# Optimization experiments

Hardware: AMD Instinct MI355X
Metric: run time of the kernel (lower is better)

## Reference

```python
import jax, jax.numpy as jnp
import numpy as np

N = 50000; E = 800000; G = 64
HID = 128; HEADS = 4; HC = HID // HEADS
L = 3; RESID_FREQ = 2
EPS = 1e-5; SLOPE = 0.2


def setup_inputs() -> dict:
    key = jax.random.key(0)
    ks = jax.random.split(key, 16)
    s = 1.0 / np.sqrt(HID)
    f = jnp.float32
    return {
        "x": jax.random.normal(ks[0], (N, HID), f),
        "edge_index": jax.random.randint(ks[1], (2, E), 0, N, dtype=jnp.int32),
        "batch": jnp.sort(jax.random.randint(ks[2], (N,), 0, G, dtype=jnp.int32)),
        "w_in1": jax.random.normal(ks[3], (HID, HID), f) * s,
        "b_in1": jnp.zeros((HID,), f),
        "w_in2": jax.random.normal(ks[4], (HID, HID), f) * s,
        "b_in2": jnp.zeros((HID,), f),
        "gat_w": jax.random.normal(ks[5], (L, HID, HID), f) * s,
        "gat_att_src": jax.random.normal(ks[6], (L, HEADS, HC), f) * s,
        "gat_att_dst": jax.random.normal(ks[7], (L, HEADS, HC), f) * s,
        "gat_b": jnp.zeros((L, HID), f),
        "gcn_w": jax.random.normal(ks[8], (L, HID, HID), f) * s,
        "gcn_b": jnp.zeros((L, HID), f),
        "norm_w": jnp.ones((L, HID), f),
        "norm_b": jnp.zeros((L, HID), f),
        "norm_ms": jnp.ones((L, HID), f),
        "skip_w": jax.random.normal(ks[9], (L, HID, HID), f) * s,
        "skip_b": jnp.zeros((L, HID), f),
        "w_h1": jax.random.normal(ks[10], (HID, HID), f) * s,
        "b_h1": jnp.zeros((HID,), f),
        "w_h2": jax.random.normal(ks[11], (HID, HID // 2), f) * s,
        "b_h2": jnp.zeros((HID // 2,), f),
        "w_h3": jax.random.normal(ks[12], (HID // 2, 1), f) * s,
        "b_h3": jnp.zeros((1,), f),
        "edge_w_param": jnp.ones((1,), f),
    }


def _gat(x, src, dst, w, a_src, a_dst, b):
    # PyG GATConv (eval): lin -> per-edge additive attention -> edge softmax over dst -> scatter-sum
    h = (x @ w).reshape(N, HEADS, HC)
    sc_src = jnp.sum(h * a_src, axis=-1)  # [N, H]
    sc_dst = jnp.sum(h * a_dst, axis=-1)
    alpha = jax.nn.leaky_relu(sc_src[src] + sc_dst[dst], SLOPE)  # [Ef, H]
    amax = jax.ops.segment_max(alpha, dst, num_segments=N)  # every node has a self-loop
    ex = jnp.exp(alpha - amax[dst])
    denom = jax.ops.segment_sum(ex, dst, num_segments=N)
    coef = ex / (denom[dst] + 1e-16)
    out = jax.ops.segment_sum(h[src] * coef[:, :, None], dst, num_segments=N)
    return out.reshape(N, HID) + b


def _gcn(x, src, dst, ew, w, b):
    # PyG GCNConv with improved=True (self-loop weight 2.0 already in ew): sym-normalized SpMM
    deg = jax.ops.segment_sum(ew, dst, num_segments=N)
    dinv = jnp.where(deg > 0, jax.lax.rsqrt(deg), 0.0)
    norm = dinv[src] * ew * dinv[dst]
    h = x @ w
    return jax.ops.segment_sum(h[src] * norm[:, None], dst, num_segments=N) + b


def _graph_norm(x, batch, w, b, ms):
    cnt = jax.ops.segment_sum(jnp.ones((N, 1), x.dtype), batch, num_segments=G)
    cnt = jnp.maximum(cnt, 1.0)
    mean = jax.ops.segment_sum(x, batch, num_segments=G) / cnt
    out = x - mean[batch] * ms
    var = jax.ops.segment_sum(out * out, batch, num_segments=G) / cnt
    return out / jnp.sqrt(var[batch] + EPS) * w + b


def reference(x, edge_index, batch, w_in1, b_in1, w_in2, b_in2, gat_w, gat_att_src,
              gat_att_dst, gat_b, gcn_w, gcn_b, norm_w, norm_b, norm_ms, skip_w,
              skip_b, w_h1, b_h1, w_h2, b_h2, w_h3, b_h3, edge_w_param):
    # undirected: concat reversed edges; then self-loops (added by both GAT and GCN convs)
    loop = jnp.arange(N, dtype=edge_index.dtype)
    src = jnp.concatenate([edge_index[0], edge_index[1], loop])
    dst = jnp.concatenate([edge_index[1], edge_index[0], loop])
    ew = jnp.concatenate([
        edge_w_param[0] * jnp.ones((2 * E,), x.dtype),
        2.0 * jnp.ones((N,), x.dtype),  # improved=True self-loop fill value
    ])
    h = jax.nn.relu(x @ w_in1 + b_in1) @ w_in2 + b_in2
    for i in range(L):
        prev = h
        g1 = _gat(h, src, dst, gat_w[i], gat_att_src[i], gat_att_dst[i], gat_b[i])
        g2 = _gcn(h, src, dst, ew, gcn_w[i], gcn_b[i])
        h = jax.nn.elu(_graph_norm(g1 + g2, batch, norm_w[i], norm_b[i], norm_ms[i]))
        if i % RESID_FREQ == 0:
            h = h + prev @ skip_w[i] + skip_b[i]
    p = jax.nn.relu(h @ w_h1 + b_h1)
    p = jax.nn.relu(p @ w_h2 + b_h2)
    return jax.nn.sigmoid(p @ w_h3 + b_h3).reshape(-1)
```

## Files before the change

### kernel.cpp

```cpp
#include <hip/hip_runtime.h>

typedef unsigned int uint;
typedef unsigned short ushort;
typedef __attribute__((ext_vector_type(8))) short short8;
typedef __attribute__((ext_vector_type(4))) float f32x4;

#define N_NODES 50000
#define N_EDGES 800000
#define ETOT    (2 * N_EDGES + N_NODES)
#define NG      64
#define NBKT    256
#define MAXB    10240
#define EPB     8192
#define NBK1    ((ETOT + EPB - 1) / EPB)
#define GSTR    320

__device__ __forceinline__ short f2bf(float f) {
  uint u = __float_as_uint(f);
  u += 0x7fffu + ((u >> 16) & 1u);
  return (short)(u >> 16);
}
__device__ __forceinline__ float bf2f(short s) {
  return __uint_as_float(((uint)(ushort)s) << 16);
}
__device__ __forceinline__ uint packbf(float a, float b) {
  return (uint)(ushort)f2bf(a) | ((uint)(ushort)f2bf(b) << 16);
}

__global__ __launch_bounds__(256) void bucket_k(const int* __restrict__ ei,
                                                int* __restrict__ gfill,
                                                uint* __restrict__ est) {
  __shared__ int hist[NBKT];
  __shared__ int cursor[NBKT];
  const int tid = threadIdx.x;
  hist[tid] = 0;
  __syncthreads();
  const int e0 = blockIdx.x * EPB;
#pragma unroll 4
  for (int i = 0; i < EPB / 256; ++i) {
    int e = e0 + i * 256 + tid;
    if (e < ETOT) {
      int d;
      if (e < N_EDGES)          d = ei[N_EDGES + e];
      else if (e < 2 * N_EDGES) d = ei[e - N_EDGES];
      else                      d = e - 2 * N_EDGES;
      atomicAdd(&hist[d >> 8], 1);
    }
  }
  __syncthreads();
  cursor[tid] = atomicAdd(&gfill[tid], hist[tid]);
  __syncthreads();
#pragma unroll 4
  for (int i = 0; i < EPB / 256; ++i) {
    int e = e0 + i * 256 + tid;
    if (e < ETOT) {
      int s, d, fl = 0;
      if (e < N_EDGES)          { s = ei[e];           d = ei[N_EDGES + e]; }
      else if (e < 2 * N_EDGES) { s = ei[e];           d = ei[e - N_EDGES]; }
      else                      { s = e - 2 * N_EDGES; d = s; fl = 1; }
      int b = d >> 8;
      int slot = atomicAdd(&cursor[b], 1);
      est[(size_t)b * MAXB + slot] = (uint)s | ((uint)(d & 255) << 16) | ((uint)fl << 24);
    }
  }
}

__global__ __launch_bounds__(256) void group_k(const int* __restrict__ gfill,
                                               const uint* __restrict__ est,
                                               const float* __restrict__ ewp,
                                               int* __restrict__ csrc,
                                               int* __restrict__ rbeg,
                                               int* __restrict__ rend,
                                               float* __restrict__ dinv) {
  __shared__ int hist[NBKT];
  __shared__ int cursor[NBKT];
  __shared__ int wsum[4];
  const int b = blockIdx.x;
  const int tid = threadIdx.x;
  const int cnt = gfill[b];
  hist[tid] = 0;
  __syncthreads();
  const uint* basep = est + (size_t)b * MAXB;
  for (int i = tid; i < cnt; i += 256)
    atomicAdd(&hist[(basep[i] >> 16) & 255], 1);
  __syncthreads();
  int v = hist[tid];
  int lane = tid & 63, wid = tid >> 6;
  int x = v;
#pragma unroll
  for (int d = 1; d < 64; d <<= 1) {
    int t = __shfl_up(x, d, 64);
    if (lane >= d) x += t;
  }
  if (lane == 63) wsum[wid] = x;
  __syncthreads();
  int woff = 0;
#pragma unroll
  for (int j = 0; j < 4; ++j) if (j < wid) woff += wsum[j];
  int excl = woff + x - v;
  cursor[tid] = excl;
  int node = b * 256 + tid;
  if (node < N_NODES) {
    int gb = b * MAXB;
    rbeg[node] = gb + excl;
    rend[node] = gb + excl + v;
    float deg = ewp[0] * (float)(v - 1) + 2.0f;
    dinv[node] = (deg > 0.f) ? rsqrtf(deg) : 0.f;
  }
  __syncthreads();
  for (int i = tid; i < cnt; i += 256) {
    uint en = basep[i];
    int dlow = (en >> 16) & 255;
    int slot = atomicAdd(&cursor[dlow], 1);
    csrc[(size_t)b * MAXB + slot] = (int)(en & 0xffffu) | (int)((en >> 24) << 31);
  }
}

__global__ __launch_bounds__(128) void gcnt_k(const int* __restrict__ batch,
                                              int* __restrict__ gcnt) {
  __shared__ int lb[NG + 1];
  int g = threadIdx.x;
  if (g <= NG) {
    int lo = 0, hi = N_NODES;
    while (lo < hi) {
      int mid = (lo + hi) >> 1;
      if (batch[mid] < g) lo = mid + 1; else hi = mid;
    }
    lb[g] = lo;
  }
  __syncthreads();
  if (g < NG) gcnt[g] = lb[g + 1] - lb[g];
}

__global__ __launch_bounds__(256) void convx_k(const float* __restrict__ x,
                                               short* __restrict__ xb) {
  int i = (blockIdx.x * 256 + threadIdx.x) * 4;
  float4 v = *(const float4*)(x + i);
  *(uint2*)(xb + i) = make_uint2(packbf(v.x, v.y), packbf(v.z, v.w));
}

__global__ __launch_bounds__(256) void prep_k(const float* __restrict__ w_in1,
                                              const float* __restrict__ w_in2,
                                              const float* __restrict__ gat_w,
                                              const float* __restrict__ gcn_w,
                                              const float* __restrict__ skip_w,
                                              const float* __restrict__ w_h1,
                                              const float* __restrict__ w_h2,
                                              short* __restrict__ WT0,
                                              short* __restrict__ WT1,
                                              short* __restrict__ WTL2,
                                              short* __restrict__ WTS,
                                              short* __restrict__ WTH1,
                                              short* __restrict__ WTH2) {
  int mat = blockIdx.x >> 2, qr = blockIdx.x & 3;
  const float* src; short* dst; int ncol = 128, dstride = 128, doff = 0;
  switch (mat) {
    case 0:  src = w_in1; dst = WT0; break;
    case 1:  src = w_in2; dst = WT1; break;
    case 2: case 3: case 4:
      src = gat_w + (size_t)(mat - 2) * 16384; dst = WTL2 + (size_t)(mat - 2) * 32768;
      dstride = 256; break;
    case 5: case 6: case 7:
      src = gcn_w + (size_t)(mat - 5) * 16384; dst = WTL2 + (size_t)(mat - 5) * 32768;
      dstride = 256; doff = 128; break;
    case 8:  src = skip_w;             dst = WTS;         break;
    case 9:  src = skip_w + 2 * 16384; dst = WTS + 16384; break;
    case 10: src = w_h1; dst = WTH1; break;
    default: src = w_h2; dst = WTH2; ncol = 64; break;
  }
  int total = 128 * ncol, chunk = total / 4;
  for (int d = qr * chunk + threadIdx.x; d < (qr + 1) * chunk; d += 256) {
    int col = d >> 7, k = d & 127;
    dst[col * dstride + doff + k] = f2bf(src[k * ncol + col]);
  }
}

__global__ __launch_bounds__(256) void attprep_k(const float* __restrict__ gat_w,
                                                 const float* __restrict__ asrc,
                                                 const float* __restrict__ adst,
                                                 const float* __restrict__ gat_b,
                                                 const float* __restrict__ gcn_b,
                                                 short* __restrict__ ATTW,
                                                 float* __restrict__ BSUM) {
  const int tid = threadIdx.x;
  for (int t = tid; t < 3072; t += 256) {
    int l = t >> 10, rem = t & 1023;
    int r = rem >> 7, k = rem & 127;
    int hd = r & 3;
    const float* av = (r < 4) ? (asrc + l * 128 + hd * 32) : (adst + l * 128 + hd * 32);
    const float* wrow = gat_w + (size_t)l * 16384 + k * 128 + hd * 32;
    float s = 0.f;
#pragma unroll
    for (int c = 0; c < 32; ++c) s = fmaf(wrow[c], av[c], s);
    ATTW[(size_t)l * 2048 + r * 128 + k] = f2bf(s);
  }
  for (int t = tid; t < 3072; t += 256)
    ATTW[(size_t)(t >> 10) * 2048 + 1024 + (t & 1023)] = 0;
  for (int t = tid; t < 384; t += 256) {
    int l = t >> 7, c = t & 127;
    BSUM[t] = gat_b[l * 128 + c] + gcn_b[l * 128 + c];
  }
}

template <int NCOL, int RELU, int ADD, int F32OUT>
__global__ __launch_bounds__(256) void bgemm_k(const short* __restrict__ A,
                                               const short* __restrict__ WT,
                                               const float* __restrict__ bias,
                                               const float* __restrict__ addsrc,
                                               short* __restrict__ outb,
                                               float* __restrict__ outf,
                                               int astr, int M) {
  constexpr int NT = NCOL / 16;
  const int lane = threadIdx.x & 63;
  const int wid = threadIdx.x >> 6;
  const int mbase = blockIdx.x * 64 + wid * 16;
  const int l15 = lane & 15, q = lane >> 4;
  int arow = mbase + l15; if (arow > M - 1) arow = M - 1;
  const short* ap = A + (size_t)arow * 128 + q * 8;
  const short* bp = WT + (size_t)l15 * 128 + q * 8;
  f32x4 acc[NT];
#pragma unroll
  for (int t = 0; t < NT; ++t) acc[t] = (f32x4)0.f;
#pragma unroll
  for (int c = 0; c < 4; ++c) {
    short8 av = *(const short8*)(ap + c * 32);
#pragma unroll
    for (int t = 0; t < NT; ++t) {
      short8 bv = *(const short8*)(bp + (size_t)t * 16 * 128 + c * 32);
      acc[t] = __builtin_amdgcn_mfma_f32_16x16x32_bf16(av, bv, acc[t], 0, 0, 0);
    }
  }
#pragma unroll
  for (int t = 0; t < NT; ++t) {
    int col = t * 16 + l15;
    float bb = bias ? bias[col] : 0.f;
#pragma unroll
    for (int r = 0; r < 4; ++r) {
      int row = mbase + q * 4 + r;
      if (row < M) {
        float v = acc[t][r] + bb;
        if (ADD) v += addsrc[(size_t)row * astr + col];
        if (RELU) v = v > 0.f ? v : 0.f;
        if (F32OUT) outf[(size_t)row * NCOL + col] = v;
        else        outb[(size_t)row * NCOL + col] = f2bf(v);
      }
    }
  }
}

__global__ __launch_bounds__(256) void agg_k(const short* __restrict__ h,
                                             const float* __restrict__ sc,
                                             const int* __restrict__ rbeg,
                                             const int* __restrict__ rend,
                                             const int* __restrict__ cs,
                                             const float* __restrict__ dinv,
                                             const float* __restrict__ ewp,
                                             short* __restrict__ A) {
  const int n = blockIdx.x * 4 + (threadIdx.x >> 6);
  const int l = threadIdx.x & 63;
  const int sub = l >> 5;
  const int f4 = l & 31;
  const float ew0 = ewp[0];
  const f32x4 sdv = *(const f32x4*)(sc + n * 16 + 4);
  const float dn = dinv[n];
  const int beg = rbeg[n], end = rend[n];
  float den[4] = {0.f, 0.f, 0.f, 0.f};
  float ag[4][4];
#pragma unroll
  for (int hd = 0; hd < 4; ++hd)
#pragma unroll
    for (int i = 0; i < 4; ++i) ag[hd][i] = 0.f;
  float ac[4] = {0.f, 0.f, 0.f, 0.f};
  for (int e0 = beg; e0 < end; e0 += 2) {
    int e = e0 + sub;
    bool valid = e < end;
    int ec = valid ? e : end - 1;
    int raw = cs[ec];
    int s = raw & 0x7fffffff;
    float w = (raw < 0) ? 2.0f : ew0;
    f32x4 ssv = *(const f32x4*)(sc + s * 16);
    float dvs = dinv[s];
    uint2 u = *(const uint2*)(h + (size_t)s * 128 + f4 * 4);
    float c2 = valid ? dvs * w * dn : 0.f;
    float v0 = __uint_as_float(u.x << 16);
    float v1 = __uint_as_float(u.x & 0xffff0000u);
    float v2 = __uint_as_float(u.y << 16);
    float v3 = __uint_as_float(u.y & 0xffff0000u);
#pragma unroll
    for (int hd = 0; hd < 4; ++hd) {
      float al = ssv[hd] + sdv[hd];
      al = fmaxf(al, 0.2f * al);
      float ex = valid ? __expf(al) : 0.f;
      den[hd] += ex;
      ag[hd][0] = fmaf(ex, v0, ag[hd][0]);
      ag[hd][1] = fmaf(ex, v1, ag[hd][1]);
      ag[hd][2] = fmaf(ex, v2, ag[hd][2]);
      ag[hd][3] = fmaf(ex, v3, ag[hd][3]);
    }
    ac[0] = fmaf(c2, v0, ac[0]);
    ac[1] = fmaf(c2, v1, ac[1]);
    ac[2] = fmaf(c2, v2, ac[2]);
    ac[3] = fmaf(c2, v3, ac[3]);
  }
#pragma unroll
  for (int hd = 0; hd < 4; ++hd) {
    den[hd] += __shfl_xor(den[hd], 32);
#pragma unroll
    for (int i = 0; i < 4; ++i) ag[hd][i] += __shfl_xor(ag[hd][i], 32);
  }
#pragma unroll
  for (int i = 0; i < 4; ++i) ac[i] += __shfl_xor(ac[i], 32);
  short* base = A + (size_t)n * 640;
  if (sub == 0) {
#pragma unroll
    for (int hd = 0; hd < 2; ++hd) {
      float inv = 1.0f / (den[hd] + 1e-16f);
      *(uint2*)(base + hd * 128 + f4 * 4) =
          make_uint2(packbf(ag[hd][0] * inv, ag[hd][1] * inv),
                     packbf(ag[hd][2] * inv, ag[hd][3] * inv));
    }
    *(uint2*)(base + 512 + f4 * 4) =
        make_uint2(packbf(ac[0], ac[1]), packbf(ac[2], ac[3]));
  } else {
#pragma unroll
    for (int hd = 2; hd < 4; ++hd) {
      float inv = 1.0f / (den[hd] + 1e-16f);
      *(uint2*)(base + hd * 128 + f4 * 4) =
          make_uint2(packbf(ag[hd][0] * inv, ag[hd][1] * inv),
                     packbf(ag[hd][2] * inv, ag[hd][3] * inv));
    }
  }
}

__global__ __launch_bounds__(256) void aggproj_k(const short* A,
                                                 const short* __restrict__ WT,
                                                 const float* __restrict__ bsum,
                                                 float* G, int M) {
  const int lane = threadIdx.x & 63;
  const int wid = threadIdx.x >> 6;
  const int mbase = blockIdx.x * 64 + wid * 16;
  const int l15 = lane & 15, q = lane >> 4;
  int arow = mbase + l15; if (arow > M - 1) arow = M - 1;
  const short* ap = A + (size_t)arow * 640 + q * 8;
  const short* bp = WT + (size_t)l15 * 256 + q * 8;
  f32x4 acc[8];
#pragma unroll
  for (int t = 0; t < 8; ++t) acc[t] = (f32x4)0.f;
  short8 avg[4];
#pragma unroll
  for (int c = 0; c < 4; ++c) avg[c] = *(const short8*)(ap + 512 + c * 32);
#pragma unroll
  for (int hd = 0; hd < 4; ++hd) {
    short8 avh[4];
#pragma unroll
    for (int c = 0; c < 4; ++c) avh[c] = *(const short8*)(ap + hd * 128 + c * 32);
#pragma unroll
    for (int tt = 0; tt < 2; ++tt) {
      int t = hd * 2 + tt;
      const short* bpt = bp + (size_t)t * 16 * 256;
#pragma unroll
      for (int c = 0; c < 4; ++c) {
        short8 bv = *(const short8*)(bpt + c * 32);
        acc[t] = __builtin_amdgcn_mfma_f32_16x16x32_bf16(avh[c], bv, acc[t], 0, 0, 0);
      }
#pragma unroll
      for (int c = 0; c < 4; ++c) {
        short8 bv = *(const short8*)(bpt + 128 + c * 32);
        acc[t] = __builtin_amdgcn_mfma_f32_16x16x32_bf16(avg[c], bv, acc[t], 0, 0, 0);
      }
    }
  }
#pragma unroll
  for (int t = 0; t < 8; ++t) {
    int col = t * 16 + l15;
    float bb = bsum[col];
#pragma unroll
    for (int r = 0; r < 4; ++r) {
      int row = mbase + q * 4 + r;
      if (row < M) G[(size_t)row * GSTR + col] = acc[t][r] + bb;
    }
  }
}

__global__ __launch_bounds__(256) void stats_k(const float* __restrict__ g,
                                               const int* __restrict__ batch,
                                               float* __restrict__ gsum) {
  int c = threadIdx.x & 127;
  int half = threadIdx.x >> 7;
  int nb = blockIdx.x * 16;
  float s = 0.f, q = 0.f;
  int curb = -1;
  for (int i = half; i < 16; i += 2) {
    int n = nb + i;
    int b = batch[n];
    if (b != curb) {
      if (curb >= 0) {
        atomicAdd(&gsum[curb * 256 + c], s);
        atomicAdd(&gsum[curb * 256 + 128 + c], q);
      }
      curb = b; s = 0.f; q = 0.f;
    }
    float v = g[(size_t)n * GSTR + c];
    s += v;
    q = fmaf(v, v, q);
  }
  if (curb >= 0) {
    atomicAdd(&gsum[curb * 256 + c], s);
    atomicAdd(&gsum[curb * 256 + 128 + c], q);
  }
}

template <int OUTBF16>
__global__ __launch_bounds__(256) void normelu_k(float* __restrict__ g,
                                                 const int* __restrict__ batch,
                                                 const float* __restrict__ gsum,
                                                 const int* __restrict__ gcnt,
                                                 const float* __restrict__ nw,
                                                 const float* __restrict__ nb_,
                                                 const float* __restrict__ nms,
                                                 short* __restrict__ outb) {
  int n = blockIdx.x * 2 + (threadIdx.x >> 7);
  int c = threadIdx.x & 127;
  int b = batch[n];
  float cntf = fmaxf((float)gcnt[b], 1.0f);
  float inv = 1.0f / cntf;
  float mean = gsum[b * 256 + c] * inv;
  float msq  = gsum[b * 256 + 128 + c] * inv;
  float ms = nms[c];
  float var = fmaxf(msq - (2.0f * ms - ms * ms) * mean * mean, 0.f);
  float v = g[(size_t)n * GSTR + c];
  float o = (v - mean * ms) * rsqrtf(var + 1e-5f) * nw[c] + nb_[c];
  o = (o > 0.f) ? o : (__expf(o) - 1.0f);
  if (OUTBF16) outb[(size_t)n * 128 + c] = f2bf(o);
  else         g[(size_t)n * GSTR + c] = o;
}

__global__ __launch_bounds__(256) void head3_k(const short* __restrict__ p2,
                                               const float* __restrict__ w3,
                                               const float* __restrict__ b3,
                                               float* __restrict__ out) {
  int n = blockIdx.x * 4 + (threadIdx.x >> 6);
  int k = threadIdx.x & 63;
  float v = bf2f(p2[(size_t)n * 64 + k]) * w3[k];
#pragma unroll
  for (int off = 32; off; off >>= 1) v += __shfl_down(v, off, 64);
  if (k == 0) out[n] = 1.0f / (1.0f + __expf(-(v + b3[0])));
}

extern "C" void kernel_launch(void* const* d_in, const int* in_sizes, int n_in,
                              void* d_out, int out_size, void* d_ws, size_t ws_size,
                              hipStream_t stream) {
  const float* x      = (const float*)d_in[0];
  const int*   ei     = (const int*)d_in[1];
  const int*   batch  = (const int*)d_in[2];
  const float* w_in1  = (const float*)d_in[3];
  const float* b_in1  = (const float*)d_in[4];
  const float* w_in2  = (const float*)d_in[5];
  const float* b_in2  = (const float*)d_in[6];
  const float* gat_w  = (const float*)d_in[7];
  const float* gat_as = (const float*)d_in[8];
  const float* gat_ad = (const float*)d_in[9];
  const float* gat_b  = (const float*)d_in[10];
  const float* gcn_w  = (const float*)d_in[11];
  const float* gcn_b  = (const float*)d_in[12];
  const float* norm_w = (const float*)d_in[13];
  const float* norm_b = (const float*)d_in[14];
  const float* norm_ms= (const float*)d_in[15];
  const float* skip_w = (const float*)d_in[16];
  const float* skip_b = (const float*)d_in[17];
  const float* w_h1   = (const float*)d_in[18];
  const float* b_h1   = (const float*)d_in[19];
  const float* w_h2   = (const float*)d_in[20];
  const float* b_h2   = (const float*)d_in[21];
  const float* w_h3   = (const float*)d_in[22];
  const float* b_h3   = (const float*)d_in[23];
  const float* ewp    = (const float*)d_in[24];
  float* out = (float*)d_out;

  char* p = (char*)d_ws;
  const size_t NBH = (size_t)N_NODES * 128 * sizeof(short);
  short* B0   = (short*)p; p += NBH;
  short* B1   = (short*)p; p += NBH;
  short* MEGA = (short*)p; p += (size_t)N_NODES * 640 * sizeof(short);
  float* G    = (float*)MEGA;
  uint*  EST  = (uint*)MEGA;
  float* SC   = (float*)p; p += (size_t)N_NODES * 16 * sizeof(float);
  int*   CSRC = (int*)p;   p += (size_t)NBKT * MAXB * sizeof(int);
  int*   RBEG = (int*)p;   p += (size_t)N_NODES * sizeof(int);
  int*   REND = (int*)p;   p += (size_t)N_NODES * sizeof(int);
  int*   GFILL= (int*)p;   p += (size_t)NBKT * sizeof(int);
  int*   GCNT = (int*)p;   p += (size_t)NG * sizeof(int);
  float* DINV = (float*)p; p += (size_t)N_NODES * sizeof(float);
  float* GSUM = (float*)p; p += (size_t)NG * 256 * sizeof(float);
  short* WT0  = (short*)p; p += 16384 * sizeof(short);
  short* WT1  = (short*)p; p += 16384 * sizeof(short);
  short* WTL2 = (short*)p; p += 3 * 32768 * sizeof(short);
  short* WTS  = (short*)p; p += 2 * 16384 * sizeof(short);
  short* WTH1 = (short*)p; p += 16384 * sizeof(short);
  short* WTH2 = (short*)p; p += 8192 * sizeof(short);
  short* ATTW = (short*)p; p += 3 * 2048 * sizeof(short);
  float* BSUM = (float*)p; p += 3 * 128 * sizeof(float);

  const int GB = (N_NODES + 63) / 64;

  hipMemsetAsync(GFILL, 0, NBKT * sizeof(int), stream);
  bucket_k<<<NBK1, 256, 0, stream>>>(ei, GFILL, EST);
  group_k<<<196, 256, 0, stream>>>(GFILL, EST, ewp, CSRC, RBEG, REND, DINV);
  gcnt_k<<<1, 128, 0, stream>>>(batch, GCNT);
  convx_k<<<(N_NODES * 128) / 1024, 256, 0, stream>>>(x, B0);
  prep_k<<<48, 256, 0, stream>>>(w_in1, w_in2, gat_w, gcn_w, skip_w, w_h1, w_h2,
                                 WT0, WT1, WTL2, WTS, WTH1, WTH2);
  attprep_k<<<1, 256, 0, stream>>>(gat_w, gat_as, gat_ad, gat_b, gcn_b, ATTW, BSUM);

  bgemm_k<128, 1, 0, 0><<<GB, 256, 0, stream>>>(B0, WT0, b_in1, nullptr, B1, nullptr, 0, N_NODES);
  bgemm_k<128, 0, 0, 0><<<GB, 256, 0, stream>>>(B1, WT1, b_in2, nullptr, B0, nullptr, 0, N_NODES);

  short* h = B0;
  for (int i = 0; i < 3; ++i) {
    short* hn = (h == B0) ? B1 : B0;
    bgemm_k<16, 0, 0, 1><<<GB, 256, 0, stream>>>(h, ATTW + (size_t)i * 2048,
                                                 nullptr, nullptr, nullptr, SC, 0, N_NODES);
    agg_k<<<N_NODES / 4, 256, 0, stream>>>(h, SC, RBEG, REND, CSRC, DINV, ewp, MEGA);
    aggproj_k<<<GB, 256, 0, stream>>>(MEGA, WTL2 + (size_t)i * 32768,
                                      BSUM + i * 128, G, N_NODES);
    hipMemsetAsync(GSUM, 0, (size_t)NG * 256 * sizeof(float), stream);
    stats_k<<<N_NODES / 16, 256, 0, stream>>>(G, batch, GSUM);
    if (i == 1) {
      normelu_k<1><<<N_NODES / 2, 256, 0, stream>>>(G, batch, GSUM, GCNT,
          norm_w + (size_t)i * 128, norm_b + (size_t)i * 128, norm_ms + (size_t)i * 128,
          hn);
    } else {
      normelu_k<0><<<N_NODES / 2, 256, 0, stream>>>(G, batch, GSUM, GCNT,
          norm_w + (size_t)i * 128, norm_b + (size_t)i * 128, norm_ms + (size_t)i * 128,
          nullptr);
      const short* wts = WTS + (size_t)(i == 0 ? 0 : 1) * 16384;
      bgemm_k<128, 0, 1, 0><<<GB, 256, 0, stream>>>(h, wts, skip_b + (size_t)i * 128,
                                                    G, hn, nullptr, GSTR, N_NODES);
    }
    h = hn;
  }

  bgemm_k<128, 1, 0, 0><<<GB, 256, 0, stream>>>(h, WTH1, b_h1, nullptr, B0, nullptr, 0, N_NODES);
  bgemm_k<64, 1, 0, 0><<<GB, 256, 0, stream>>>(B0, WTH2, b_h2, nullptr, MEGA, nullptr, 0, N_NODES);
  head3_k<<<N_NODES / 4, 256, 0, stream>>>(MEGA, w_h3, b_h3, out);
}
```

Baseline: 962.1 us.

## Process four edges per wave in GAT/GCN aggregation and batch GSUM memsets

The aggregation kernel now handles four edges per iteration, one per 16-lane group. Lanes 0-15 compute the per-head attention exponent and GCN coefficient once per edge-head and broadcast them by shuffle, so the exponent is no longer recomputed redundantly in every lane. Each lane then loads 16 bytes of the source feature row and accumulates with packed 2-wide float math, followed by a two-step cross-group reduction. Separately, the three per-layer GSUM buffers are zeroed in a single memset together with GFILL, removing the per-layer memset calls. The trade-off is more shuffles, higher register pressure from the 40 float accumulators, and idle lanes during the score phase.

New measurement: 1.020 ms. +6.0%, slower.

```diff
diff --git a/kernel.cpp b/kernel.cpp
--- a/kernel.cpp
+++ b/kernel.cpp
@@ -4,6 +4,7 @@
 typedef unsigned short ushort;
 typedef __attribute__((ext_vector_type(8))) short short8;
 typedef __attribute__((ext_vector_type(4))) float f32x4;
+typedef __attribute__((ext_vector_type(2))) float f32x2;
 
 #define N_NODES 50000
 #define N_EDGES 800000
@@ -25,6 +26,12 @@
 }
 __device__ __forceinline__ uint packbf(float a, float b) {
   return (uint)(ushort)f2bf(a) | ((uint)(ushort)f2bf(b) << 16);
+}
+__device__ __forceinline__ f32x2 unpk2(uint u) {
+  f32x2 r;
+  r.x = __uint_as_float(u << 16);
+  r.y = __uint_as_float(u & 0xffff0000u);
+  return r;
 }
 
 __global__ __launch_bounds__(256) void bucket_k(const int* __restrict__ ei,
@@ -258,77 +265,99 @@
                                              short* __restrict__ A) {
   const int n = blockIdx.x * 4 + (threadIdx.x >> 6);
   const int l = threadIdx.x & 63;
-  const int sub = l >> 5;
-  const int f4 = l & 31;
+  const int sub = l >> 4;
+  const int l15 = l & 15;
+  const int chd = l & 3;
   const float ew0 = ewp[0];
-  const f32x4 sdv = *(const f32x4*)(sc + n * 16 + 4);
   const float dn = dinv[n];
+  const float sd = sc[n * 16 + 4 + chd];
   const int beg = rbeg[n], end = rend[n];
-  float den[4] = {0.f, 0.f, 0.f, 0.f};
-  float ag[4][4];
+  f32x2 ag[4][4], ac[4];
 #pragma unroll
   for (int hd = 0; hd < 4; ++hd)
 #pragma unroll
-    for (int i = 0; i < 4; ++i) ag[hd][i] = 0.f;
-  float ac[4] = {0.f, 0.f, 0.f, 0.f};
-  for (int e0 = beg; e0 < end; e0 += 2) {
-    int e = e0 + sub;
-    bool valid = e < end;
-    int ec = valid ? e : end - 1;
-    int raw = cs[ec];
-    int s = raw & 0x7fffffff;
-    float w = (raw < 0) ? 2.0f : ew0;
-    f32x4 ssv = *(const f32x4*)(sc + s * 16);
-    float dvs = dinv[s];
-    uint2 u = *(const uint2*)(h + (size_t)s * 128 + f4 * 4);
-    float c2 = valid ? dvs * w * dn : 0.f;
-    float v0 = __uint_as_float(u.x << 16);
-    float v1 = __uint_as_float(u.x & 0xffff0000u);
-    float v2 = __uint_as_float(u.y << 16);
-    float v3 = __uint_as_float(u.y & 0xffff0000u);
+    for (int j = 0; j < 4; ++j) ag[hd][j] = (f32x2)0.f;
+#pragma unroll
+  for (int j = 0; j < 4; ++j) ac[j] = (f32x2)0.f;
+  float denp = 0.f;
+
+  for (int e0 = beg; e0 < end; e0 += 4) {
+    float ex = 0.f, c2 = 0.f; int s = 0;
+    if (l < 16) {
+      int e = e0 + (l >> 2);
+      int ec = (e < end) ? e : end - 1;
+      int raw = cs[ec];
+      s = raw & 0x7fffffff;
+      float w = (raw < 0) ? 2.0f : ew0;
+      float ss = sc[s * 16 + chd];
+      float al = ss + sd;
+      al = fmaxf(al, 0.2f * al);
+      bool valid = e < end;
+      ex = valid ? __expf(al) : 0.f;
+      c2 = valid ? dinv[s] * w * dn : 0.f;
+      denp += ex;
+    }
+    int ssub = __shfl(s, sub * 4, 64);
+    float ex0 = __shfl(ex, sub * 4 + 0, 64);
+    float ex1 = __shfl(ex, sub * 4 + 1, 64);
+    float ex2 = __shfl(ex, sub * 4 + 2, 64);
+    float ex3 = __shfl(ex, sub * 4 + 3, 64);
+    float c2v = __shfl(c2, sub * 4, 64);
+    uint4 u = *(const uint4*)(h + (size_t)ssub * 128 + l15 * 8);
+    f32x2 v0 = unpk2(u.x), v1 = unpk2(u.y), v2 = unpk2(u.z), v3 = unpk2(u.w);
+    f32x2 e2;
+    e2.x = ex0; e2.y = ex0;
+    ag[0][0] += e2 * v0; ag[0][1] += e2 * v1; ag[0][2] += e2 * v2; ag[0][3] += e2 * v3;
+    e2.x = ex1; e2.y = ex1;
+    ag[1][0] += e2 * v0; ag[1][1] += e2 * v1; ag[1][2] += e2 * v2; ag[1][3] += e2 * v3;
+    e2.x = ex2; e2.y = ex2;
+    ag[2][0] += e2 * v0; ag[2][1] += e2 * v1; ag[2][2] += e2 * v2; ag[2][3] += e2 * v3;
+    e2.x = ex3; e2.y = ex3;
+    ag[3][0] += e2 * v0; ag[3][1] += e2 * v1; ag[3][2] += e2 * v2; ag[3][3] += e2 * v3;
+    e2.x = c2v; e2.y = c2v;
+    ac[0] += e2 * v0; ac[1] += e2 * v1; ac[2] += e2 * v2; ac[3] += e2 * v3;
+  }
+
+  denp += __shfl_xor(denp, 4, 64);
+  denp += __shfl_xor(denp, 8, 64);
+#pragma unroll
+  for (int hd = 0; hd < 4; ++hd)
+#pragma unroll
+    for (int j = 0; j < 4; ++j) {
+      f32x2 t = ag[hd][j];
+      t.x += __shfl_xor(t.x, 16, 64); t.y += __shfl_xor(t.y, 16, 64);
+      t.x += __shfl_xor(t.x, 32, 64); t.y += __shfl_xor(t.y, 32, 64);
+      ag[hd][j] = t;
+    }
+#pragma unroll
+  for (int j = 0; j < 4; ++j) {
+    f32x2 t = ac[j];
+    t.x += __shfl_xor(t.x, 16, 64); t.y += __shfl_xor(t.y, 16, 64);
+    t.x += __shfl_xor(t.x, 32, 64); t.y += __shfl_xor(t.y, 32, 64);
+    ac[j] = t;
+  }
+  float dh0 = __shfl(denp, 0, 64), dh1 = __shfl(denp, 1, 64);
+  float dh2 = __shfl(denp, 2, 64), dh3 = __shfl(denp, 3, 64);
+  if (l < 16) {
+    short* base = A + (size_t)n * 640;
+    float invd[4] = {1.0f / (dh0 + 1e-16f), 1.0f / (dh1 + 1e-16f),
+                     1.0f / (dh2 + 1e-16f), 1.0f / (dh3 + 1e-16f)};
 #pragma unroll
     for (int hd = 0; hd < 4; ++hd) {
-      float al = ssv[hd] + sdv[hd];
-      al = fmaxf(al, 0.2f * al);
-      float ex = valid ? __expf(al) : 0.f;
-      den[hd] += ex;
-      ag[hd][0] = fmaf(ex, v0, ag[hd][0]);
-      ag[hd][1] = fmaf(ex, v1, ag[hd][1]);
-      ag[hd][2] = fmaf(ex, v2, ag[hd][2]);
-      ag[hd][3] = fmaf(ex, v3, ag[hd][3]);
-    }
-    ac[0] = fmaf(c2, v0, ac[0]);
-    ac[1] = fmaf(c2, v1, ac[1]);
-    ac[2] = fmaf(c2, v2, ac[2]);
-    ac[3] = fmaf(c2, v3, ac[3]);
-  }
-#pragma unroll
-  for (int hd = 0; hd < 4; ++hd) {
-    den[hd] += __shfl_xor(den[hd], 32);
-#pragma unroll
-    for (int i = 0; i < 4; ++i) ag[hd][i] += __shfl_xor(ag[hd][i], 32);
-  }
-#pragma unroll
-  for (int i = 0; i < 4; ++i) ac[i] += __shfl_xor(ac[i], 32);
-  short* base = A + (size_t)n * 640;
-  if (sub == 0) {
-#pragma unroll
-    for (int hd = 0; hd < 2; ++hd) {
-      float inv = 1.0f / (den[hd] + 1e-16f);
-      *(uint2*)(base + hd * 128 + f4 * 4) =
-          make_uint2(packbf(ag[hd][0] * inv, ag[hd][1] * inv),
-                     packbf(ag[hd][2] * inv, ag[hd][3] * inv));
-    }
-    *(uint2*)(base + 512 + f4 * 4) =
-        make_uint2(packbf(ac[0], ac[1]), packbf(ac[2], ac[3]));
-  } else {
-#pragma unroll
-    for (int hd = 2; hd < 4; ++hd) {
-      float inv = 1.0f / (den[hd] + 1e-16f);
-      *(uint2*)(base + hd * 128 + f4 * 4) =
-          make_uint2(packbf(ag[hd][0] * inv, ag[hd][1] * inv),
-                     packbf(ag[hd][2] * inv, ag[hd][3] * inv));
-    }
+      float iv = invd[hd];
+      uint4 o;
+      o.x = packbf(ag[hd][0].x * iv, ag[hd][0].y * iv);
+      o.y = packbf(ag[hd][1].x * iv, ag[hd][1].y * iv);
+      o.z = packbf(ag[hd][2].x * iv, ag[hd][2].y * iv);
+      o.w = packbf(ag[hd][3].x * iv, ag[hd][3].y * iv);
+      *(uint4*)(base + hd * 128 + l15 * 8) = o;
+    }
+    uint4 o;
+    o.x = packbf(ac[0].x, ac[0].y);
+    o.y = packbf(ac[1].x, ac[1].y);
+    o.z = packbf(ac[2].x, ac[2].y);
+    o.w = packbf(ac[3].x, ac[3].y);
+    *(uint4*)(base + 512 + l15 * 8) = o;
   }
 }
 
@@ -488,10 +517,12 @@
   int*   CSRC = (int*)p;   p += (size_t)NBKT * MAXB * sizeof(int);
   int*   RBEG = (int*)p;   p += (size_t)N_NODES * sizeof(int);
   int*   REND = (int*)p;   p += (size_t)N_NODES * sizeof(int);
+  char*  zbase = p;
   int*   GFILL= (int*)p;   p += (size_t)NBKT * sizeof(int);
+  float* GSUM = (float*)p; p += (size_t)3 * NG * 256 * sizeof(float);
+  size_t znb  = (size_t)((char*)p - zbase);
   int*   GCNT = (int*)p;   p += (size_t)NG * sizeof(int);
   float* DINV = (float*)p; p += (size_t)N_NODES * sizeof(float);
-  float* GSUM = (float*)p; p += (size_t)NG * 256 * sizeof(float);
   short* WT0  = (short*)p; p += 16384 * sizeof(short);
   short* WT1  = (short*)p; p += 16384 * sizeof(short);
   short* WTL2 = (short*)p; p += 3 * 32768 * sizeof(short);
@@ -503,7 +534,7 @@
 
   const int GB = (N_NODES + 63) / 64;
 
-  hipMemsetAsync(GFILL, 0, NBKT * sizeof(int), stream);
+  hipMemsetAsync(zbase, 0, znb, stream);
   bucket_k<<<NBK1, 256, 0, stream>>>(ei, GFILL, EST);
   group_k<<<196, 256, 0, stream>>>(GFILL, EST, ewp, CSRC, RBEG, REND, DINV);
   gcnt_k<<<1, 128, 0, stream>>>(batch, GCNT);
@@ -518,19 +549,19 @@
   short* h = B0;
   for (int i = 0; i < 3; ++i) {
     short* hn = (h == B0) ? B1 : B0;
+    float* gsum_i = GSUM + (size_t)i * NG * 256;
     bgemm_k<16, 0, 0, 1><<<GB, 256, 0, stream>>>(h, ATTW + (size_t)i * 2048,
                                                  nullptr, nullptr, nullptr, SC, 0, N_NODES);
     agg_k<<<N_NODES / 4, 256, 0, stream>>>(h, SC, RBEG, REND, CSRC, DINV, ewp, MEGA);
     aggproj_k<<<GB, 256, 0, stream>>>(MEGA, WTL2 + (size_t)i * 32768,
                                       BSUM + i * 128, G, N_NODES);
-    hipMemsetAsync(GSUM, 0, (size_t)NG * 256 * sizeof(float), stream);
-    stats_k<<<N_NODES / 16, 256, 0, stream>>>(G, batch, GSUM);
+    stats_k<<<N_NODES / 16, 256, 0, stream>>>(G, batch, gsum_i);
     if (i == 1) {
-      normelu_k<1><<<N_NODES / 2, 256, 0, stream>>>(G, batch, GSUM, GCNT,
+      normelu_k<1><<<N_NODES / 2, 256, 0, stream>>>(G, batch, gsum_i, GCNT,
           norm_w + (size_t)i * 128, norm_b + (size_t)i * 128, norm_ms + (size_t)i * 128,
           hn);
     } else {
-      normelu_k<0><<<N_NODES / 2, 256, 0, stream>>>(G, batch, GSUM, GCNT,
+      normelu_k<0><<<N_NODES / 2, 256, 0, stream>>>(G, batch, gsum_i, GCNT,
           norm_w + (size_t)i * 128, norm_b + (size_t)i * 128, norm_ms + (size_t)i * 128,
           nullptr);
       const short* wts = WTS + (size_t)(i == 0 ? 0 : 1) * 16384;
```

## Precompute normalized edge attention coefficients in compact edge array before aggregation

Applied to the files above, without the earlier changes.

Adds a coef_k pass that computes per-edge GAT softmax weights (normalized) and GCN coefficients, packs them as fp16 along with the source index into a dense 12-byte-per-edge array, so agg_k no longer gathers scores, dinv and recomputes exp per feature lane. CSR storage is compacted via a bucket prefix scan instead of fixed MAXB strides. GSUM buffers are allocated per layer and zeroed by a single memset up front. It adds an extra kernel and edge-array traffic per layer, and fp16 coefficients plus a 16-bit packed source index may lose precision or range (N=50000 fits in 16 bits).

Result: slower. 984.4 us (+2.3%).

```diff
diff --git a/kernel.cpp b/kernel.cpp
--- a/kernel.cpp
+++ b/kernel.cpp
@@ -1,4 +1,5 @@
 #include <hip/hip_runtime.h>
+#include <hip/hip_fp16.h>
 
 typedef unsigned int uint;
 typedef unsigned short ushort;
@@ -25,6 +26,14 @@
 }
 __device__ __forceinline__ uint packbf(float a, float b) {
   return (uint)(ushort)f2bf(a) | ((uint)(ushort)f2bf(b) << 16);
+}
+__device__ __forceinline__ uint pkh2(float a, float b) {
+  __half2 h = __floats2half2_rn(a, b);
+  return *(uint*)&h;
+}
+__device__ __forceinline__ float2 uph2(uint u) {
+  __half2 h = *(__half2*)&u;
+  return __half22float2(h);
 }
 
 __global__ __launch_bounds__(256) void bucket_k(const int* __restrict__ ei,
@@ -65,7 +74,27 @@
   }
 }
 
+__global__ __launch_bounds__(256) void bktscan_k(const int* __restrict__ gfill,
+                                                 int* __restrict__ bktbase) {
+  __shared__ int wsum[4];
+  int tid = threadIdx.x, lane = tid & 63, wid = tid >> 6;
+  int v = gfill[tid];
+  int x = v;
+#pragma unroll
+  for (int d = 1; d < 64; d <<= 1) {
+    int t = __shfl_up(x, d, 64);
+    if (lane >= d) x += t;
+  }
+  if (lane == 63) wsum[wid] = x;
+  __syncthreads();
+  int woff = 0;
+#pragma unroll
+  for (int j = 0; j < 4; ++j) if (j < wid) woff += wsum[j];
+  bktbase[tid] = woff + x - v;
+}
+
 __global__ __launch_bounds__(256) void group_k(const int* __restrict__ gfill,
+                                               const int* __restrict__ bktbase,
                                                const uint* __restrict__ est,
                                                const float* __restrict__ ewp,
                                                int* __restrict__ csrc,
@@ -78,6 +107,7 @@
   const int b = blockIdx.x;
   const int tid = threadIdx.x;
   const int cnt = gfill[b];
+  const int gb = bktbase[b];
   hist[tid] = 0;
   __syncthreads();
   const uint* basep = est + (size_t)b * MAXB;
@@ -101,7 +131,6 @@
   cursor[tid] = excl;
   int node = b * 256 + tid;
   if (node < N_NODES) {
-    int gb = b * MAXB;
     rbeg[node] = gb + excl;
     rend[node] = gb + excl + v;
     float deg = ewp[0] * (float)(v - 1) + 2.0f;
@@ -112,7 +141,7 @@
     uint en = basep[i];
     int dlow = (en >> 16) & 255;
     int slot = atomicAdd(&cursor[dlow], 1);
-    csrc[(size_t)b * MAXB + slot] = (int)(en & 0xffffu) | (int)((en >> 24) << 31);
+    csrc[gb + slot] = (int)(en & 0xffffu) | (int)((en >> 24) << 31);
   }
 }
 
@@ -248,86 +277,119 @@
   }
 }
 
+__global__ __launch_bounds__(256) void coef_k(const float* __restrict__ sc,
+                                              const int* __restrict__ rbeg,
+                                              const int* __restrict__ rend,
+                                              const int* __restrict__ cs,
+                                              const float* __restrict__ dinv,
+                                              const float* __restrict__ ewp,
+                                              uint* __restrict__ COEF) {
+  const int n = blockIdx.x * 4 + (threadIdx.x >> 6);
+  const int l = threadIdx.x & 63;
+  const float ew0 = ewp[0];
+  const float dn = dinv[n];
+  const f32x4 sdv = *(const f32x4*)(sc + n * 16 + 4);
+  const int beg = rbeg[n], end = rend[n];
+  float den0 = 0.f, den1 = 0.f, den2 = 0.f, den3 = 0.f;
+  for (int e = beg + l; e < end; e += 64) {
+    int raw = cs[e];
+    int s = raw & 0x7fffffff;
+    float w = (raw < 0) ? 2.0f : ew0;
+    f32x4 ssv = *(const f32x4*)(sc + (size_t)s * 16);
+    float a0 = ssv[0] + sdv[0]; a0 = fmaxf(a0, 0.2f * a0);
+    float a1 = ssv[1] + sdv[1]; a1 = fmaxf(a1, 0.2f * a1);
+    float a2 = ssv[2] + sdv[2]; a2 = fmaxf(a2, 0.2f * a2);
+    float a3 = ssv[3] + sdv[3]; a3 = fmaxf(a3, 0.2f * a3);
+    float e0 = __expf(a0), e1 = __expf(a1), e2 = __expf(a2), e3 = __expf(a3);
+    den0 += e0; den1 += e1; den2 += e2; den3 += e3;
+    float c2 = dinv[s] * w * dn;
+    uint* cp = COEF + (size_t)e * 3;
+    cp[0] = pkh2(e0, e1);
+    cp[1] = pkh2(e2, e3);
+    __half hc = __float2half(c2);
+    cp[2] = (uint)(*(ushort*)&hc) | ((uint)s << 16);
+  }
+#pragma unroll
+  for (int off = 32; off; off >>= 1) {
+    den0 += __shfl_xor(den0, off, 64);
+    den1 += __shfl_xor(den1, off, 64);
+    den2 += __shfl_xor(den2, off, 64);
+    den3 += __shfl_xor(den3, off, 64);
+  }
+  float i0 = 1.0f / (den0 + 1e-16f), i1 = 1.0f / (den1 + 1e-16f);
+  float i2 = 1.0f / (den2 + 1e-16f), i3 = 1.0f / (den3 + 1e-16f);
+  for (int e = beg + l; e < end; e += 64) {
+    uint* cp = COEF + (size_t)e * 3;
+    float2 p01 = uph2(cp[0]);
+    float2 p23 = uph2(cp[1]);
+    cp[0] = pkh2(p01.x * i0, p01.y * i1);
+    cp[1] = pkh2(p23.x * i2, p23.y * i3);
+  }
+}
+
 __global__ __launch_bounds__(256) void agg_k(const short* __restrict__ h,
-                                             const float* __restrict__ sc,
+                                             const uint* __restrict__ COEF,
                                              const int* __restrict__ rbeg,
                                              const int* __restrict__ rend,
-                                             const int* __restrict__ cs,
-                                             const float* __restrict__ dinv,
-                                             const float* __restrict__ ewp,
                                              short* __restrict__ A) {
   const int n = blockIdx.x * 4 + (threadIdx.x >> 6);
   const int l = threadIdx.x & 63;
   const int sub = l >> 5;
   const int f4 = l & 31;
-  const float ew0 = ewp[0];
-  const f32x4 sdv = *(const f32x4*)(sc + n * 16 + 4);
-  const float dn = dinv[n];
   const int beg = rbeg[n], end = rend[n];
-  float den[4] = {0.f, 0.f, 0.f, 0.f};
-  float ag[4][4];
+  float ag[4][4], ac[4];
 #pragma unroll
   for (int hd = 0; hd < 4; ++hd)
 #pragma unroll
     for (int i = 0; i < 4; ++i) ag[hd][i] = 0.f;
-  float ac[4] = {0.f, 0.f, 0.f, 0.f};
+#pragma unroll
+  for (int i = 0; i < 4; ++i) ac[i] = 0.f;
   for (int e0 = beg; e0 < end; e0 += 2) {
     int e = e0 + sub;
-    bool valid = e < end;
-    int ec = valid ? e : end - 1;
-    int raw = cs[ec];
-    int s = raw & 0x7fffffff;
-    float w = (raw < 0) ? 2.0f : ew0;
-    f32x4 ssv = *(const f32x4*)(sc + s * 16);
-    float dvs = dinv[s];
+    int ec = (e < end) ? e : ETOT;
+    const uint* cp = COEF + (size_t)ec * 3;
+    uint c0 = cp[0], c1 = cp[1], c2w = cp[2];
+    int s = (int)(c2w >> 16);
+    float2 p01 = uph2(c0);
+    float2 p23 = uph2(c1);
+    ushort hc = (ushort)(c2w & 0xffffu);
+    float c2 = __half2float(*(__half*)&hc);
     uint2 u = *(const uint2*)(h + (size_t)s * 128 + f4 * 4);
-    float c2 = valid ? dvs * w * dn : 0.f;
     float v0 = __uint_as_float(u.x << 16);
     float v1 = __uint_as_float(u.x & 0xffff0000u);
     float v2 = __uint_as_float(u.y << 16);
     float v3 = __uint_as_float(u.y & 0xffff0000u);
-#pragma unroll
-    for (int hd = 0; hd < 4; ++hd) {
-      float al = ssv[hd] + sdv[hd];
-      al = fmaxf(al, 0.2f * al);
-      float ex = valid ? __expf(al) : 0.f;
-      den[hd] += ex;
-      ag[hd][0] = fmaf(ex, v0, ag[hd][0]);
-      ag[hd][1] = fmaf(ex, v1, ag[hd][1]);
-      ag[hd][2] = fmaf(ex, v2, ag[hd][2]);
-      ag[hd][3] = fmaf(ex, v3, ag[hd][3]);
-    }
-    ac[0] = fmaf(c2, v0, ac[0]);
-    ac[1] = fmaf(c2, v1, ac[1]);
-    ac[2] = fmaf(c2, v2, ac[2]);
-    ac[3] = fmaf(c2, v3, ac[3]);
-  }
-#pragma unroll
-  for (int hd = 0; hd < 4; ++hd) {
-    den[hd] += __shfl_xor(den[hd], 32);
+    ag[0][0] = fmaf(p01.x, v0, ag[0][0]); ag[0][1] = fmaf(p01.x, v1, ag[0][1]);
+    ag[0][2] = fmaf(p01.x, v2, ag[0][2]); ag[0][3] = fmaf(p01.x, v3, ag[0][3]);
+    ag[1][0] = fmaf(p01.y, v0, ag[1][0]); ag[1][1] = fmaf(p01.y, v1, ag[1][1]);
+    ag[1][2] = fmaf(p01.y, v2, ag[1][2]); ag[1][3] = fmaf(p01.y, v3, ag[1][3]);
+    ag[2][0] = fmaf(p23.x, v0, ag[2][0]); ag[2][1] = fmaf(p23.x, v1, ag[2][1]);
+    ag[2][2] = fmaf(p23.x, v2, ag[2][2]); ag[2][3] = fmaf(p23.x, v3, ag[2][3]);
+    ag[3][0] = fmaf(p23.y, v0, ag[3][0]); ag[3][1] = fmaf(p23.y, v1, ag[3][1]);
+    ag[3][2] = fmaf(p23.y, v2, ag[3][2]); ag[3][3] = fmaf(p23.y, v3, ag[3][3]);
+    ac[0] = fmaf(c2, v0, ac[0]); ac[1] = fmaf(c2, v1, ac[1]);
+    ac[2] = fmaf(c2, v2, ac[2]); ac[3] = fmaf(c2, v3, ac[3]);
+  }
+#pragma unroll
+  for (int hd = 0; hd < 4; ++hd)
 #pragma unroll
     for (int i = 0; i < 4; ++i) ag[hd][i] += __shfl_xor(ag[hd][i], 32);
-  }
 #pragma unroll
   for (int i = 0; i < 4; ++i) ac[i] += __shfl_xor(ac[i], 32);
   short* base = A + (size_t)n * 640;
   if (sub == 0) {
 #pragma unroll
     for (int hd = 0; hd < 2; ++hd) {
-      float inv = 1.0f / (den[hd] + 1e-16f);
       *(uint2*)(base + hd * 128 + f4 * 4) =
-          make_uint2(packbf(ag[hd][0] * inv, ag[hd][1] * inv),
-                     packbf(ag[hd][2] * inv, ag[hd][3] * inv));
+          make_uint2(packbf(ag[hd][0], ag[hd][1]), packbf(ag[hd][2], ag[hd][3]));
     }
     *(uint2*)(base + 512 + f4 * 4) =
         make_uint2(packbf(ac[0], ac[1]), packbf(ac[2], ac[3]));
   } else {
 #pragma unroll
     for (int hd = 2; hd < 4; ++hd) {
-      float inv = 1.0f / (den[hd] + 1e-16f);
       *(uint2*)(base + hd * 128 + f4 * 4) =
-          make_uint2(packbf(ag[hd][0] * inv, ag[hd][1] * inv),
-                     packbf(ag[hd][2] * inv, ag[hd][3] * inv));
+          make_uint2(packbf(ag[hd][0], ag[hd][1]), packbf(ag[hd][2], ag[hd][3]));
     }
   }
 }
@@ -485,13 +547,17 @@
   float* G    = (float*)MEGA;
   uint*  EST  = (uint*)MEGA;
   float* SC   = (float*)p; p += (size_t)N_NODES * 16 * sizeof(float);
-  int*   CSRC = (int*)p;   p += (size_t)NBKT * MAXB * sizeof(int);
+  int*   CSRC = (int*)p;   p += (size_t)ETOT * sizeof(int);
+  uint*  COEF = (uint*)p;  p += (size_t)(ETOT + 1) * 3 * sizeof(uint);
   int*   RBEG = (int*)p;   p += (size_t)N_NODES * sizeof(int);
   int*   REND = (int*)p;   p += (size_t)N_NODES * sizeof(int);
+  char*  zbase = p;
   int*   GFILL= (int*)p;   p += (size_t)NBKT * sizeof(int);
+  float* GSUM = (float*)p; p += (size_t)3 * NG * 256 * sizeof(float);
+  size_t znb  = (size_t)((char*)p - zbase);
+  int*   BKTB = (int*)p;   p += (size_t)NBKT * sizeof(int);
   int*   GCNT = (int*)p;   p += (size_t)NG * sizeof(int);
   float* DINV = (float*)p; p += (size_t)N_NODES * sizeof(float);
-  float* GSUM = (float*)p; p += (size_t)NG * 256 * sizeof(float);
   short* WT0  = (short*)p; p += 16384 * sizeof(short);
   short* WT1  = (short*)p; p += 16384 * sizeof(short);
   short* WTL2 = (short*)p; p += 3 * 32768 * sizeof(short);
@@ -503,9 +569,11 @@
 
   const int GB = (N_NODES + 63) / 64;
 
-  hipMemsetAsync(GFILL, 0, NBKT * sizeof(int), stream);
+  hipMemsetAsync(zbase, 0, znb, stream);
+  hipMemsetAsync(COEF + (size_t)ETOT * 3, 0, 12, stream);
   bucket_k<<<NBK1, 256, 0, stream>>>(ei, GFILL, EST);
-  group_k<<<196, 256, 0, stream>>>(GFILL, EST, ewp, CSRC, RBEG, REND, DINV);
+  bktscan_k<<<1, 256, 0, stream>>>(GFILL, BKTB);
+  group_k<<<196, 256, 0, stream>>>(GFILL, BKTB, EST, ewp, CSRC, RBEG, REND, DINV);
   gcnt_k<<<1, 128, 0, stream>>>(batch, GCNT);
   convx_k<<<(N_NODES * 128) / 1024, 256, 0, stream>>>(x, B0);
   prep_k<<<48, 256, 0, stream>>>(w_in1, w_in2, gat_w, gcn_w, skip_w, w_h1, w_h2,
@@ -518,19 +586,20 @@
   short* h = B0;
   for (int i = 0; i < 3; ++i) {
     short* hn = (h == B0) ? B1 : B0;
+    float* gsum_i = GSUM + (size_t)i * NG * 256;
     bgemm_k<16, 0, 0, 1><<<GB, 256, 0, stream>>>(h, ATTW + (size_t)i * 2048,
                                                  nullptr, nullptr, nullptr, SC, 0, N_NODES);
-    agg_k<<<N_NODES / 4, 256, 0, stream>>>(h, SC, RBEG, REND, CSRC, DINV, ewp, MEGA);
+    coef_k<<<N_NODES / 4, 256, 0, stream>>>(SC, RBEG, REND, CSRC, DINV, ewp, COEF);
+    agg_k<<<N_NODES / 4, 256, 0, stream>>>(h, COEF, RBEG, REND, MEGA);
     aggproj_k<<<GB, 256, 0, stream>>>(MEGA, WTL2 + (size_t)i * 32768,
                                       BSUM + i * 128, G, N_NODES);
-    hipMemsetAsync(GSUM, 0, (size_t)NG * 256 * sizeof(float), stream);
-    stats_k<<<N_NODES / 16, 256, 0, stream>>>(G, batch, GSUM);
+    stats_k<<<N_NODES / 16, 256, 0, stream>>>(G, batch, gsum_i);
     if (i == 1) {
-      normelu_k<1><<<N_NODES / 2, 256, 0, stream>>>(G, batch, GSUM, GCNT,
+      normelu_k<1><<<N_NODES / 2, 256, 0, stream>>>(G, batch, gsum_i, GCNT,
           norm_w + (size_t)i * 128, norm_b + (size_t)i * 128, norm_ms + (size_t)i * 128,
           hn);
     } else {
-      normelu_k<0><<<N_NODES / 2, 256, 0, stream>>>(G, batch, GSUM, GCNT,
+      normelu_k<0><<<N_NODES / 2, 256, 0, stream>>>(G, batch, gsum_i, GCNT,
           norm_w + (size_t)i * 128, norm_b + (size_t)i * 128, norm_ms + (size_t)i * 128,
           nullptr);
       const short* wts = WTS + (size_t)(i == 0 ? 0 : 1) * 16384;
```
